# Optimization experiments

Hardware: AMD Instinct MI355X
Metric: run time of the kernel (lower is better)

Reference implementation:

```python
import jax, jax.numpy as jnp
import numpy as np

CURRENT_TIME = 1000.0
TIME_WEIGHT = 0.1
NEG_INF = -1e9


def setup_inputs() -> dict:
    key = jax.random.key(0)
    ks = jax.random.split(key, 7)
    B, M, D, C = 1024, 65536, 64, 16
    return {
        "query": jax.random.normal(ks[0], (B, D), dtype=jnp.float32),
        "context": jax.random.normal(ks[1], (B, C), dtype=jnp.float32),
        "mem_keys": jax.random.normal(ks[2], (M, D), dtype=jnp.float32) * 0.1,
        "mem_values": jax.random.normal(ks[3], (M, D), dtype=jnp.float32) * 0.1,
        "mem_contexts": jax.random.normal(ks[4], (M, C), dtype=jnp.float32) * 0.1,
        "mem_timestamps": jax.random.uniform(ks[5], (M, 1), dtype=jnp.float32) * CURRENT_TIME,
        "used_mask": jax.random.randint(ks[6], (M,), 0, 2) > 0,
    }


def reference(query, context, mem_keys, mem_values, mem_contexts, mem_timestamps, used_mask):
    # content score: [B, M]
    scores = jnp.einsum("bd,md->bm", query, mem_keys)
    # context score, scaled by 0.5
    scores = scores + 0.5 * jnp.einsum("bc,mc->bm", context, mem_contexts)
    # time-decay bias, scaled by 0.3 (broadcast over batch)
    decay = jnp.exp(-TIME_WEIGHT * (CURRENT_TIME - mem_timestamps[:, 0]))  # [M]
    scores = scores + 0.3 * decay[None, :]
    # unused slots get -1e9 exactly as torch.full init
    scores = jnp.where(used_mask[None, :], scores, NEG_INF)
    attn = jax.nn.softmax(scores, axis=-1)
    return jnp.einsum("bm,md->bd", attn, mem_values)
```

## Files before the change

kernel.cpp:

```cpp
#include <hip/hip_runtime.h>

typedef float f32x4 __attribute__((ext_vector_type(4)));
typedef __bf16 bf16x8 __attribute__((ext_vector_type(8)));
typedef unsigned int u32;
typedef unsigned short u16;

#define MTOT 65536
#define BTOT 1024
#define DD 64
#define LOG2E 1.44269504088896340736f
#define MFMA __builtin_amdgcn_mfma_f32_16x16x32_bf16

#define NROWBLK ((MTOT + BTOT) * 24 / 256)
#define NVTBLK  (MTOT / 64)
#define ESPACE  (DD * BTOT + BTOT)
#define NSLICE  8

__device__ __forceinline__ u16 f2bf(float f) { return __builtin_bit_cast(u16, (__bf16)f); }
__device__ __forceinline__ u32 pk2(float a, float b) {
    return (u32)f2bf(a) | ((u32)f2bf(b) << 16);
}
__device__ __forceinline__ bf16x8 ldg8(const u16* p) { return *reinterpret_cast<const bf16x8*>(p); }
__device__ __forceinline__ void glds16(const void* g, void* l) {
    __builtin_amdgcn_global_load_lds((const __attribute__((address_space(1))) u32*)g,
                                     (__attribute__((address_space(3))) u32*)l, 16, 0, 0);
}

__global__ __launch_bounds__(256)
void prep_all(const float* __restrict__ q, const float* __restrict__ ctx,
              const float* __restrict__ K, const float* __restrict__ CT,
              const float* __restrict__ TS, const int* __restrict__ mask,
              const float* __restrict__ V,
              u16* __restrict__ Qc, u16* __restrict__ KC, u16* __restrict__ Vt)
{
    __shared__ u16 L[64][68];
    const int blk = blockIdx.x, t = threadIdx.x;

    if (blk < NROWBLK) {
        const int R = MTOT + BTOT;
        int gid = blk * 256 + t;
        float4 v = {0.f, 0.f, 0.f, 0.f};
        u16* dst;
        if (gid < R * 16) {
            int row = gid >> 4, qd = gid & 15;
            bool isQ = row >= MTOT;
            int r2 = isQ ? row - MTOT : row;
            v = *reinterpret_cast<const float4*>((isQ ? q : K) + (size_t)r2 * 64 + qd * 4);
            if (isQ) { v.x *= LOG2E; v.y *= LOG2E; v.z *= LOG2E; v.w *= LOG2E; }
            dst = (isQ ? Qc : KC) + (size_t)r2 * 96 + qd * 4;
        } else if (gid < R * 20) {
            int i = gid - R * 16;
            int row = i >> 2, qd = i & 3;
            bool isQ = row >= MTOT;
            int r2 = isQ ? row - MTOT : row;
            v = *reinterpret_cast<const float4*>((isQ ? ctx : CT) + (size_t)r2 * 16 + qd * 4);
            if (isQ) { const float s = 0.5f * LOG2E; v.x *= s; v.y *= s; v.z *= s; v.w *= s; }
            dst = (isQ ? Qc : KC) + (size_t)r2 * 96 + 64 + qd * 4;
        } else {
            int i = gid - R * 20;
            int row = i >> 2, qd = i & 3;
            bool isQ = row >= MTOT;
            int r2 = isQ ? row - MTOT : row;
            if (qd == 0)
                v.x = isQ ? LOG2E
                          : (mask[r2] ? 0.3f * __expf(-0.1f * (1000.0f - TS[r2])) : -100.0f);
            dst = (isQ ? Qc : KC) + (size_t)r2 * 96 + 80 + qd * 4;
        }
        ushort4 o = { f2bf(v.x), f2bf(v.y), f2bf(v.z), f2bf(v.w) };
        *reinterpret_cast<ushort4*>(dst) = o;
        return;
    }

    const int m0 = (blk - NROWBLK) * 64;
#pragma unroll
    for (int p = 0; p < 4; ++p) {
        int fi = t + p * 256;
        int mi = fi >> 4, di = (fi & 15) << 2;
        float4 v = *reinterpret_cast<const float4*>(V + (size_t)(m0 + mi) * 64 + di);
        ushort4 o = { f2bf(v.x), f2bf(v.y), f2bf(v.z), f2bf(v.w) };
        *reinterpret_cast<ushort4*>(&L[mi][di]) = o;
    }
    __syncthreads();
    const int d = t >> 2, seg = t & 3;
    u32 pk[8];
#pragma unroll
    for (int pr = 0; pr < 8; ++pr) {
        int c0 = seg * 16 + pr * 2;
        int g32 = c0 >> 5;
        int i0 = c0 & 31, i1 = (c0 + 1) & 31;
        int mp0 = g32 * 32 + (i0 >> 1) + (i0 & 1) * 16;
        int mp1 = g32 * 32 + (i1 >> 1) + (i1 & 1) * 16;
        pk[pr] = (u32)L[mp0][d] | ((u32)L[mp1][d] << 16);
    }
    uint4 A = {pk[0], pk[1], pk[2], pk[3]}, B4 = {pk[4], pk[5], pk[6], pk[7]};
    u16* dst = Vt + (size_t)d * MTOT + m0 + seg * 16;
    *reinterpret_cast<uint4*>(dst)     = A;
    *reinterpret_cast<uint4*>(dst + 8) = B4;
}

__global__ __launch_bounds__(256, 3)
void epmem_mfma(const u16* __restrict__ Qc, const u16* __restrict__ KCg,
                const u16* __restrict__ Vtg,
                float* __restrict__ pl, float* __restrict__ pacc,
                int mper, int NB)
{
    __shared__ __align__(16) u16 KCs[2][64 * 96];
    __shared__ __align__(16) u16 Vts[2][64 * 64];
    __shared__ __align__(16) u16 Pb[4][32][40];

    const int tid = threadIdx.x;
    const int w = tid >> 6, lane = tid & 63;
    const int l15 = lane & 15, g = lane >> 4;

    const int bid = blockIdx.x;
    const int o = (bid & 7) * (NB >> 3) + (bid >> 3);
    const int rt = o & 7, ch = o >> 3;
    const int rbase = rt * 128 + w * 32;

    const u16* q0 = Qc + (size_t)(rbase + l15) * 96 + g * 8;
    const bf16x8 qf00 = ldg8(q0), qf01 = ldg8(q0 + 32), qf02 = ldg8(q0 + 64);
    const u16* q1 = q0 + 16 * 96;
    const bf16x8 qf10 = ldg8(q1), qf11 = ldg8(q1 + 32), qf12 = ldg8(q1 + 64);

    const int m0 = ch * mper;
    const int m1 = (m0 + mper < MTOT) ? (m0 + mper) : MTOT;
    const int ntiles = (m1 > m0) ? ((m1 - m0) >> 6) : 0;

    int kgo[3];
#pragma unroll
    for (int i = 0; i < 3; ++i) {
        int ol = w * 3072 + i * 1024 + lane * 16;
        int row = ol / 192;
        int c = (ol - row * 192) >> 4;
        int u = (c < 8) ? (c ^ (row & 7)) : (8 + ((c & 3) ^ (row & 3)));
        kgo[i] = row * 192 + u * 16;
    }
    int vgo[2];
#pragma unroll
    for (int i = 0; i < 2; ++i) {
        int ol = w * 2048 + i * 1024 + lane * 16;
        int row = ol >> 7, c = (ol >> 4) & 7;
        int u = c ^ (row & 7);
        vgo[i] = row * (MTOT * 2) + u * 16;
    }

    f32x4 a00 = {0,0,0,0}, a01 = {0,0,0,0}, a02 = {0,0,0,0}, a03 = {0,0,0,0};
    f32x4 a10 = {0,0,0,0}, a11 = {0,0,0,0}, a12 = {0,0,0,0}, a13 = {0,0,0,0};
    float ls[8] = {0,0,0,0,0,0,0,0};

    if (ntiles > 0) {
        const char* kb = (const char*)KCg + (size_t)m0 * 192;
        const char* vb = (const char*)Vtg + (size_t)m0 * 2;
#pragma unroll
        for (int i = 0; i < 3; ++i) glds16(kb + kgo[i], (char*)KCs[0] + w * 3072 + i * 1024);
#pragma unroll
        for (int i = 0; i < 2; ++i) glds16(vb + vgo[i], (char*)Vts[0] + w * 2048 + i * 1024);
    }
    __syncthreads();

    char* pbw = (char*)Pb[w];
    const int xr = l15 & 7;
    const int x3 = l15 & 3;

    int cur = 0;
    for (int t = 0; t < ntiles; ++t) {
        if (t + 1 < ntiles) {
            int mt = m0 + ((t + 1) << 6);
            const char* kb = (const char*)KCg + (size_t)mt * 192;
            const char* vb = (const char*)Vtg + (size_t)mt * 2;
            int nb = cur ^ 1;
#pragma unroll
            for (int i = 0; i < 3; ++i) glds16(kb + kgo[i], (char*)KCs[nb] + w * 3072 + i * 1024);
#pragma unroll
            for (int i = 0; i < 2; ++i) glds16(vb + vgo[i], (char*)Vts[nb] + w * 2048 + i * 1024);
        }
        const char* kcb = (const char*)KCs[cur];
        const char* vtb = (const char*)Vts[cur];

#pragma unroll
        for (int j = 0; j < 2; ++j) {
            bf16x8 kf[2][3];
#pragma unroll
            for (int s = 0; s < 2; ++s) {
                int row = j * 32 + s * 16 + l15;
                kf[s][0] = *reinterpret_cast<const bf16x8*>(kcb + row * 192 + (((0 + g) ^ xr) << 4));
                kf[s][1] = *reinterpret_cast<const bf16x8*>(kcb + row * 192 + (((4 + g) ^ xr) << 4));
                kf[s][2] = *reinterpret_cast<const bf16x8*>(kcb + row * 192 + ((8 + (g ^ x3)) << 4));
            }
            bf16x8 vf[4];
#pragma unroll
            for (int d4 = 0; d4 < 4; ++d4) {
                int row = d4 * 16 + l15;
                vf[d4] = *reinterpret_cast<const bf16x8*>(vtb + row * 128 + (((j * 4 + g) ^ xr) << 4));
            }

            f32x4 S00 = {0,0,0,0}, S01 = {0,0,0,0}, S10 = {0,0,0,0}, S11 = {0,0,0,0};
            S00 = MFMA(qf00, kf[0][0], S00,0,0,0); S00 = MFMA(qf01, kf[0][1], S00,0,0,0); S00 = MFMA(qf02, kf[0][2], S00,0,0,0);
            S01 = MFMA(qf00, kf[1][0], S01,0,0,0); S01 = MFMA(qf01, kf[1][1], S01,0,0,0); S01 = MFMA(qf02, kf[1][2], S01,0,0,0);
            S10 = MFMA(qf10, kf[0][0], S10,0,0,0); S10 = MFMA(qf11, kf[0][1], S10,0,0,0); S10 = MFMA(qf12, kf[0][2], S10,0,0,0);
            S11 = MFMA(qf10, kf[1][0], S11,0,0,0); S11 = MFMA(qf11, kf[1][1], S11,0,0,0); S11 = MFMA(qf12, kf[1][2], S11,0,0,0);

#pragma unroll
            for (int r = 0; r < 4; ++r) {
                float p00 = exp2f(S00[r]), p01 = exp2f(S01[r]);
                float p10 = exp2f(S10[r]), p11 = exp2f(S11[r]);
                ls[r]     += p00 + p01;
                ls[4 + r] += p10 + p11;
                int row0 = g * 4 + r, row1 = 16 + g * 4 + r;
                int cw = (((l15 >> 2) ^ r) << 4) | ((l15 & 3) << 2);
                *(u32*)(pbw + row0 * 80 + cw) = pk2(p00, p01);
                *(u32*)(pbw + row1 * 80 + cw) = pk2(p10, p11);
            }
            bf16x8 pa0 = *reinterpret_cast<const bf16x8*>(pbw + l15 * 80        + ((g ^ x3) << 4));
            bf16x8 pa1 = *reinterpret_cast<const bf16x8*>(pbw + (16 + l15) * 80 + ((g ^ x3) << 4));

            a00 = MFMA(pa0, vf[0], a00,0,0,0); a01 = MFMA(pa0, vf[1], a01,0,0,0);
            a02 = MFMA(pa0, vf[2], a02,0,0,0); a03 = MFMA(pa0, vf[3], a03,0,0,0);
            a10 = MFMA(pa1, vf[0], a10,0,0,0); a11 = MFMA(pa1, vf[1], a11,0,0,0);
            a12 = MFMA(pa1, vf[2], a12,0,0,0); a13 = MFMA(pa1, vf[3], a13,0,0,0);
        }
        __syncthreads();
        cur ^= 1;
    }

#pragma unroll
    for (int i = 0; i < 8; ++i) {
        float v = ls[i];
        v += __shfl_xor(v, 1, 16); v += __shfl_xor(v, 2, 16);
        v += __shfl_xor(v, 4, 16); v += __shfl_xor(v, 8, 16);
        ls[i] = v;
    }
    if (l15 == 0) {
        f32x4 s0 = {ls[0], ls[1], ls[2], ls[3]};
        f32x4 s1 = {ls[4], ls[5], ls[6], ls[7]};
        *reinterpret_cast<f32x4*>(pl + (size_t)ch * BTOT + rbase + g * 4)      = s0;
        *reinterpret_cast<f32x4*>(pl + (size_t)ch * BTOT + rbase + 16 + g * 4) = s1;
    }

    float* b0 = pacc + ((size_t)ch * DD + l15) * BTOT + rbase + g * 4;
    *reinterpret_cast<f32x4*>(b0 + (size_t)0  * BTOT) = a00;
    *reinterpret_cast<f32x4*>(b0 + (size_t)16 * BTOT) = a01;
    *reinterpret_cast<f32x4*>(b0 + (size_t)32 * BTOT) = a02;
    *reinterpret_cast<f32x4*>(b0 + (size_t)48 * BTOT) = a03;
    float* b1 = b0 + 16;
    *reinterpret_cast<f32x4*>(b1 + (size_t)0  * BTOT) = a10;
    *reinterpret_cast<f32x4*>(b1 + (size_t)16 * BTOT) = a11;
    *reinterpret_cast<f32x4*>(b1 + (size_t)32 * BTOT) = a12;
    *reinterpret_cast<f32x4*>(b1 + (size_t)48 * BTOT) = a13;
}

__global__ __launch_bounds__(256)
void combineA(const float* __restrict__ pl, const float* __restrict__ pacc,
              float* __restrict__ part, int cper)
{
    int e = blockIdx.x * 256 + threadIdx.x;
    int s = blockIdx.y;
    int c0 = s * cper;
    float v0 = 0.f, v1 = 0.f;
    if (e < DD * BTOT) {
        const float* p = pacc + (size_t)c0 * (DD * BTOT) + e;
#pragma unroll 2
        for (int i = 0; i + 1 < cper; i += 2) {
            v0 += p[(size_t)i * (DD * BTOT)];
            v1 += p[(size_t)(i + 1) * (DD * BTOT)];
        }
        if (cper & 1) v0 += p[(size_t)(cper - 1) * (DD * BTOT)];
    } else {
        const float* p = pl + (size_t)c0 * BTOT + (e - DD * BTOT);
#pragma unroll 2
        for (int i = 0; i + 1 < cper; i += 2) {
            v0 += p[(size_t)i * BTOT];
            v1 += p[(size_t)(i + 1) * BTOT];
        }
        if (cper & 1) v0 += p[(size_t)(cper - 1) * BTOT];
    }
    part[(size_t)s * ESPACE + e] = v0 + v1;
}

__global__ __launch_bounds__(256)
void combineB(const float* __restrict__ part, float* __restrict__ out)
{
    int t = blockIdx.x * 256 + threadIdx.x;
    int d = t >> 10, b = t & 1023;
    float v = 0.f, lssum = 0.f;
#pragma unroll
    for (int s = 0; s < NSLICE; ++s) {
        v     += part[(size_t)s * ESPACE + t];
        lssum += part[(size_t)s * ESPACE + DD * BTOT + b];
    }
    out[(size_t)b * DD + d] = v / lssum;
}

extern "C" void kernel_launch(void* const* d_in, const int* in_sizes, int n_in,
                              void* d_out, int out_size, void* d_ws, size_t ws_size,
                              hipStream_t stream)
{
    const float* q    = (const float*)d_in[0];
    const float* ctx  = (const float*)d_in[1];
    const float* K    = (const float*)d_in[2];
    const float* V    = (const float*)d_in[3];
    const float* CT   = (const float*)d_in[4];
    const float* TS   = (const float*)d_in[5];
    const int*   mask = (const int*)d_in[6];

    char* wsb = (char*)d_ws;
    u16* Qc = (u16*)(wsb);
    u16* KC = (u16*)(wsb + 196608);
    u16* Vt = (u16*)(wsb + 196608 + 12582912);
    size_t fixed = 196608 + 12582912 + 8388608;

    size_t chunk = (size_t)BTOT * (DD + 1) * sizeof(float);
    size_t partB = (size_t)NSLICE * ESPACE * sizeof(float);
    int SPLIT = (int)((ws_size - fixed - partB) / chunk);
    if (SPLIT > 96) SPLIT = 96;
    SPLIT &= ~7;
    if (SPLIT < 8) SPLIT = 8;

    float* pl   = (float*)(wsb + fixed);
    float* pacc = pl + (size_t)SPLIT * BTOT;
    float* part = pacc + (size_t)SPLIT * DD * BTOT;

    int mper = ((MTOT + SPLIT - 1) / SPLIT + 63) & ~63;
    int cper = SPLIT / NSLICE;

    prep_all<<<NROWBLK + NVTBLK, 256, 0, stream>>>(q, ctx, K, CT, TS, mask, V, Qc, KC, Vt);

    int NB = 8 * SPLIT;
    epmem_mfma<<<NB, 256, 0, stream>>>(Qc, KC, Vt, pl, pacc, mper, NB);

    dim3 gA((ESPACE + 255) / 256, NSLICE);
    combineA<<<gA, 256, 0, stream>>>(pl, pacc, part, cper);
    combineB<<<(DD * BTOT) / 256, 256, 0, stream>>>(part, (float*)d_out);
}
```

Measured before the change: 63.15 us.

## Double rows per wave, compute softmax row sums via MFMA ones-vector

Each wave now handles 64 query rows instead of 32, so every K/V tile loaded into shared memory feeds twice as many rows. Fewer row tiles per chunk lets the memory split grow and the grid shrink accordingly. Row sums of exp scores now come from an extra MFMA against a ones vector instead of scalar adds and shuffles, and exp2 uses the hardware builtin. The cost is more accumulator registers, which lowers the occupancy bound to 2 blocks per CU, and sums taken from bf16-rounded probabilities.

```diff
diff --git a/kernel.cpp b/kernel.cpp
--- a/kernel.cpp
+++ b/kernel.cpp
@@ -21,6 +21,13 @@
     return (u32)f2bf(a) | ((u32)f2bf(b) << 16);
 }
 __device__ __forceinline__ bf16x8 ldg8(const u16* p) { return *reinterpret_cast<const bf16x8*>(p); }
+__device__ __forceinline__ float fexp2(float x) {
+#if __has_builtin(__builtin_amdgcn_exp2f)
+    return __builtin_amdgcn_exp2f(x);
+#else
+    return exp2f(x);
+#endif
+}
 __device__ __forceinline__ void glds16(const void* g, void* l) {
     __builtin_amdgcn_global_load_lds((const __attribute__((address_space(1))) u32*)g,
                                      (__attribute__((address_space(3))) u32*)l, 16, 0, 0);
@@ -98,7 +105,7 @@
     *reinterpret_cast<uint4*>(dst + 8) = B4;
 }
 
-__global__ __launch_bounds__(256, 3)
+__global__ __launch_bounds__(256, 2)
 void epmem_mfma(const u16* __restrict__ Qc, const u16* __restrict__ KCg,
                 const u16* __restrict__ Vtg,
                 float* __restrict__ pl, float* __restrict__ pacc,
@@ -114,13 +121,16 @@
 
     const int bid = blockIdx.x;
     const int o = (bid & 7) * (NB >> 3) + (bid >> 3);
-    const int rt = o & 7, ch = o >> 3;
-    const int rbase = rt * 128 + w * 32;
-
-    const u16* q0 = Qc + (size_t)(rbase + l15) * 96 + g * 8;
-    const bf16x8 qf00 = ldg8(q0), qf01 = ldg8(q0 + 32), qf02 = ldg8(q0 + 64);
-    const u16* q1 = q0 + 16 * 96;
-    const bf16x8 qf10 = ldg8(q1), qf11 = ldg8(q1 + 32), qf12 = ldg8(q1 + 64);
+    const int rt = o & 3, ch = o >> 2;
+    const int rbase = rt * 256 + w * 64;
+
+    const u16* qp = Qc + (size_t)(rbase + l15) * 96 + g * 8;
+    bf16x8 qf[4][3];
+#pragma unroll
+    for (int sb = 0; sb < 4; ++sb)
+#pragma unroll
+        for (int c = 0; c < 3; ++c)
+            qf[sb][c] = ldg8(qp + sb * 16 * 96 + c * 32);
 
     const int m0 = ch * mper;
     const int m1 = (m0 + mper < MTOT) ? (m0 + mper) : MTOT;
@@ -144,9 +154,18 @@
         vgo[i] = row * (MTOT * 2) + u * 16;
     }
 
-    f32x4 a00 = {0,0,0,0}, a01 = {0,0,0,0}, a02 = {0,0,0,0}, a03 = {0,0,0,0};
-    f32x4 a10 = {0,0,0,0}, a11 = {0,0,0,0}, a12 = {0,0,0,0}, a13 = {0,0,0,0};
-    float ls[8] = {0,0,0,0,0,0,0,0};
+    const u32 ow = (l15 == 0) ? 0x3F803F80u : 0u;
+    const uint4 ou = {ow, ow, ow, ow};
+    const bf16x8 onesf = __builtin_bit_cast(bf16x8, ou);
+
+    f32x4 acc[4][4];
+    f32x4 accl[4];
+#pragma unroll
+    for (int sb = 0; sb < 4; ++sb) {
+        accl[sb] = (f32x4){0, 0, 0, 0};
+#pragma unroll
+        for (int d4 = 0; d4 < 4; ++d4) acc[sb][d4] = (f32x4){0, 0, 0, 0};
+    }
 
     if (ntiles > 0) {
         const char* kb = (const char*)KCg + (size_t)m0 * 192;
@@ -194,59 +213,50 @@
                 vf[d4] = *reinterpret_cast<const bf16x8*>(vtb + row * 128 + (((j * 4 + g) ^ xr) << 4));
             }
 
-            f32x4 S00 = {0,0,0,0}, S01 = {0,0,0,0}, S10 = {0,0,0,0}, S11 = {0,0,0,0};
-            S00 = MFMA(qf00, kf[0][0], S00,0,0,0); S00 = MFMA(qf01, kf[0][1], S00,0,0,0); S00 = MFMA(qf02, kf[0][2], S00,0,0,0);
-            S01 = MFMA(qf00, kf[1][0], S01,0,0,0); S01 = MFMA(qf01, kf[1][1], S01,0,0,0); S01 = MFMA(qf02, kf[1][2], S01,0,0,0);
-            S10 = MFMA(qf10, kf[0][0], S10,0,0,0); S10 = MFMA(qf11, kf[0][1], S10,0,0,0); S10 = MFMA(qf12, kf[0][2], S10,0,0,0);
-            S11 = MFMA(qf10, kf[1][0], S11,0,0,0); S11 = MFMA(qf11, kf[1][1], S11,0,0,0); S11 = MFMA(qf12, kf[1][2], S11,0,0,0);
-
-#pragma unroll
-            for (int r = 0; r < 4; ++r) {
-                float p00 = exp2f(S00[r]), p01 = exp2f(S01[r]);
-                float p10 = exp2f(S10[r]), p11 = exp2f(S11[r]);
-                ls[r]     += p00 + p01;
-                ls[4 + r] += p10 + p11;
-                int row0 = g * 4 + r, row1 = 16 + g * 4 + r;
-                int cw = (((l15 >> 2) ^ r) << 4) | ((l15 & 3) << 2);
-                *(u32*)(pbw + row0 * 80 + cw) = pk2(p00, p01);
-                *(u32*)(pbw + row1 * 80 + cw) = pk2(p10, p11);
+#pragma unroll
+            for (int h = 0; h < 2; ++h) {
+                f32x4 S00 = {0,0,0,0}, S01 = {0,0,0,0}, S10 = {0,0,0,0}, S11 = {0,0,0,0};
+                S00 = MFMA(qf[2*h][0],   kf[0][0], S00,0,0,0); S00 = MFMA(qf[2*h][1],   kf[0][1], S00,0,0,0); S00 = MFMA(qf[2*h][2],   kf[0][2], S00,0,0,0);
+                S01 = MFMA(qf[2*h][0],   kf[1][0], S01,0,0,0); S01 = MFMA(qf[2*h][1],   kf[1][1], S01,0,0,0); S01 = MFMA(qf[2*h][2],   kf[1][2], S01,0,0,0);
+                S10 = MFMA(qf[2*h+1][0], kf[0][0], S10,0,0,0); S10 = MFMA(qf[2*h+1][1], kf[0][1], S10,0,0,0); S10 = MFMA(qf[2*h+1][2], kf[0][2], S10,0,0,0);
+                S11 = MFMA(qf[2*h+1][0], kf[1][0], S11,0,0,0); S11 = MFMA(qf[2*h+1][1], kf[1][1], S11,0,0,0); S11 = MFMA(qf[2*h+1][2], kf[1][2], S11,0,0,0);
+
+#pragma unroll
+                for (int r = 0; r < 4; ++r) {
+                    float p00 = fexp2(S00[r]), p01 = fexp2(S01[r]);
+                    float p10 = fexp2(S10[r]), p11 = fexp2(S11[r]);
+                    int row0 = g * 4 + r, row1 = 16 + g * 4 + r;
+                    int cw = (((l15 >> 2) ^ r) << 4) | ((l15 & 3) << 2);
+                    *(u32*)(pbw + row0 * 80 + cw) = pk2(p00, p01);
+                    *(u32*)(pbw + row1 * 80 + cw) = pk2(p10, p11);
+                }
+                bf16x8 pa0 = *reinterpret_cast<const bf16x8*>(pbw + l15 * 80        + ((g ^ x3) << 4));
+                bf16x8 pa1 = *reinterpret_cast<const bf16x8*>(pbw + (16 + l15) * 80 + ((g ^ x3) << 4));
+
+                acc[2*h][0]   = MFMA(pa0, vf[0], acc[2*h][0],0,0,0);   acc[2*h][1]   = MFMA(pa0, vf[1], acc[2*h][1],0,0,0);
+                acc[2*h][2]   = MFMA(pa0, vf[2], acc[2*h][2],0,0,0);   acc[2*h][3]   = MFMA(pa0, vf[3], acc[2*h][3],0,0,0);
+                acc[2*h+1][0] = MFMA(pa1, vf[0], acc[2*h+1][0],0,0,0); acc[2*h+1][1] = MFMA(pa1, vf[1], acc[2*h+1][1],0,0,0);
+                acc[2*h+1][2] = MFMA(pa1, vf[2], acc[2*h+1][2],0,0,0); acc[2*h+1][3] = MFMA(pa1, vf[3], acc[2*h+1][3],0,0,0);
+                accl[2*h]   = MFMA(pa0, onesf, accl[2*h],0,0,0);
+                accl[2*h+1] = MFMA(pa1, onesf, accl[2*h+1],0,0,0);
             }
-            bf16x8 pa0 = *reinterpret_cast<const bf16x8*>(pbw + l15 * 80        + ((g ^ x3) << 4));
-            bf16x8 pa1 = *reinterpret_cast<const bf16x8*>(pbw + (16 + l15) * 80 + ((g ^ x3) << 4));
-
-            a00 = MFMA(pa0, vf[0], a00,0,0,0); a01 = MFMA(pa0, vf[1], a01,0,0,0);
-            a02 = MFMA(pa0, vf[2], a02,0,0,0); a03 = MFMA(pa0, vf[3], a03,0,0,0);
-            a10 = MFMA(pa1, vf[0], a10,0,0,0); a11 = MFMA(pa1, vf[1], a11,0,0,0);
-            a12 = MFMA(pa1, vf[2], a12,0,0,0); a13 = MFMA(pa1, vf[3], a13,0,0,0);
         }
         __syncthreads();
         cur ^= 1;
     }
 
-#pragma unroll
-    for (int i = 0; i < 8; ++i) {
-        float v = ls[i];
-        v += __shfl_xor(v, 1, 16); v += __shfl_xor(v, 2, 16);
-        v += __shfl_xor(v, 4, 16); v += __shfl_xor(v, 8, 16);
-        ls[i] = v;
-    }
     if (l15 == 0) {
-        f32x4 s0 = {ls[0], ls[1], ls[2], ls[3]};
-        f32x4 s1 = {ls[4], ls[5], ls[6], ls[7]};
-        *reinterpret_cast<f32x4*>(pl + (size_t)ch * BTOT + rbase + g * 4)      = s0;
-        *reinterpret_cast<f32x4*>(pl + (size_t)ch * BTOT + rbase + 16 + g * 4) = s1;
-    }
-
-    float* b0 = pacc + ((size_t)ch * DD + l15) * BTOT + rbase + g * 4;
-    *reinterpret_cast<f32x4*>(b0 + (size_t)0  * BTOT) = a00;
-    *reinterpret_cast<f32x4*>(b0 + (size_t)16 * BTOT) = a01;
-    *reinterpret_cast<f32x4*>(b0 + (size_t)32 * BTOT) = a02;
-    *reinterpret_cast<f32x4*>(b0 + (size_t)48 * BTOT) = a03;
-    float* b1 = b0 + 16;
-    *reinterpret_cast<f32x4*>(b1 + (size_t)0  * BTOT) = a10;
-    *reinterpret_cast<f32x4*>(b1 + (size_t)16 * BTOT) = a11;
-    *reinterpret_cast<f32x4*>(b1 + (size_t)32 * BTOT) = a12;
-    *reinterpret_cast<f32x4*>(b1 + (size_t)48 * BTOT) = a13;
+#pragma unroll
+        for (int sb = 0; sb < 4; ++sb)
+            *reinterpret_cast<f32x4*>(pl + (size_t)ch * BTOT + rbase + sb * 16 + g * 4) = accl[sb];
+    }
+
+    float* bp = pacc + ((size_t)ch * DD + l15) * BTOT + rbase + g * 4;
+#pragma unroll
+    for (int sb = 0; sb < 4; ++sb)
+#pragma unroll
+        for (int d4 = 0; d4 < 4; ++d4)
+            *reinterpret_cast<f32x4*>(bp + (size_t)(d4 * 16) * BTOT + sb * 16) = acc[sb][d4];
 }
 
 __global__ __launch_bounds__(256)
@@ -312,7 +322,7 @@
     size_t chunk = (size_t)BTOT * (DD + 1) * sizeof(float);
     size_t partB = (size_t)NSLICE * ESPACE * sizeof(float);
     int SPLIT = (int)((ws_size - fixed - partB) / chunk);
-    if (SPLIT > 96) SPLIT = 96;
+    if (SPLIT > 128) SPLIT = 128;
     SPLIT &= ~7;
     if (SPLIT < 8) SPLIT = 8;
 
@@ -325,7 +335,7 @@
 
     prep_all<<<NROWBLK + NVTBLK, 256, 0, stream>>>(q, ctx, K, CT, TS, mask, V, Qc, KC, Vt);
 
-    int NB = 8 * SPLIT;
+    int NB = 4 * SPLIT;
     epmem_mfma<<<NB, 256, 0, stream>>>(Qc, KC, Vt, pl, pacc, mper, NB);
 
     dim3 gA((ESPACE + 255) / 256, NSLICE);
```

Result: faster. 56.01 us (-11.3%).
